# Optimization experiments

Measured on AMD Instinct MI355X. Metric: run time of the kernel, lower is better.

## Reference

```python
import jax, jax.numpy as jnp
import numpy as np

B, S, T = 32, 64, 64          # batch, src_len, tgt_len
E = 1024                      # embedding_dim
H = 512                       # encoder hidden per direction
H2 = 2 * H                    # decoder hidden = enc_output_dim = 1024
VS, VT = 32000, 32000         # src / tgt vocab
L_ENC, L_DEC = 2, 2


def setup_inputs() -> dict:
    key = jax.random.key(0)
    ks = jax.random.split(key, 16)
    s = 0.05
    return {
        # tokens in [1, V) -> no pad tokens, all src_lens == S
        "x": jax.random.randint(ks[0], (B, S), 1, VS),
        "y": jax.random.randint(ks[1], (B, T), 1, VT),
        "src_emb": jax.random.normal(ks[2], (VS, E), jnp.float32) * s,
        "tgt_emb": jax.random.normal(ks[3], (VT, E), jnp.float32) * s,
        # encoder weights: [layer, dir(0=fwd,1=bwd), 4H, in] with in = E = 2H
        "enc_W_ih": jax.random.normal(ks[4], (L_ENC, 2, 4 * H, E), jnp.float32) * s,
        "enc_W_hh": jax.random.normal(ks[5], (L_ENC, 2, 4 * H, H), jnp.float32) * s,
        "enc_b_ih": jax.random.normal(ks[6], (L_ENC, 2, 4 * H), jnp.float32) * s,
        "enc_b_hh": jax.random.normal(ks[7], (L_ENC, 2, 4 * H), jnp.float32) * s,
        # decoder LSTMCells: cell0 input = E + H2 = 2048, cell1 input = H2
        "dec_W_ih0": jax.random.normal(ks[8], (4 * H2, E + H2), jnp.float32) * s,
        "dec_W_ih1": jax.random.normal(ks[9], (4 * H2, H2), jnp.float32) * s,
        "dec_W_hh": jax.random.normal(ks[10], (L_DEC, 4 * H2, H2), jnp.float32) * s,
        "dec_b_ih": jax.random.normal(ks[11], (L_DEC, 4 * H2), jnp.float32) * s,
        "dec_b_hh": jax.random.normal(ks[12], (L_DEC, 4 * H2), jnp.float32) * s,
        "W_out": jax.random.normal(ks[13], (VT, H2), jnp.float32) * s,
        "b_out": jax.random.normal(ks[14], (VT,), jnp.float32) * s,
    }


def _lstm_cell(x, h, c, W_ih, W_hh, b):
    # PyTorch gate order: i, f, g, o
    gates = x @ W_ih.T + h @ W_hh.T + b
    i, f, g, o = jnp.split(gates, 4, axis=-1)
    c2 = jax.nn.sigmoid(f) * c + jax.nn.sigmoid(i) * jnp.tanh(g)
    h2 = jax.nn.sigmoid(o) * jnp.tanh(c2)
    return h2, c2


def _run_dir(xseq, W_ih, W_hh, b):
    # xseq: [T, B, D] -> outputs [T, B, H], final (h, c)
    Bn, Hn = xseq.shape[1], W_hh.shape[1]
    init = (jnp.zeros((Bn, Hn), xseq.dtype), jnp.zeros((Bn, Hn), xseq.dtype))
    def step(carry, xt):
        h, c = carry
        h2, c2 = _lstm_cell(xt, h, c, W_ih, W_hh, b)
        return (h2, c2), h2
    (hT, cT), ys = jax.lax.scan(step, init, xseq)
    return ys, hT, cT


def _forward(x, y, src_emb, tgt_emb, enc_W_ih, enc_W_hh, enc_b_ih, enc_b_hh,
             dec_W_ih0, dec_W_ih1, dec_W_hh, dec_b_ih, dec_b_hh, W_out, b_out):
    # All src lengths are full -> per-row flip == full flip (pack is a no-op).
    x_rev = jnp.flip(x, axis=1)
    seq = src_emb[x_rev].transpose(1, 0, 2)  # [S, B, E]; dropout=0 (eval)

    h_fin, c_fin = [], []
    for l in range(L_ENC):
        b_f = enc_b_ih[l, 0] + enc_b_hh[l, 0]
        b_b = enc_b_ih[l, 1] + enc_b_hh[l, 1]
        ys_f, hT_f, cT_f = _run_dir(seq, enc_W_ih[l, 0], enc_W_hh[l, 0], b_f)
        ys_b, hT_b, cT_b = _run_dir(seq[::-1], enc_W_ih[l, 1], enc_W_hh[l, 1], b_b)
        seq = jnp.concatenate([ys_f, ys_b[::-1]], axis=-1)  # [S, B, 2H]
        h_fin.append(jnp.concatenate([hT_f, hT_b], axis=-1))  # [B, 2H]
        c_fin.append(jnp.concatenate([cT_f, cT_b], axis=-1))

    context = h_fin[-1]  # cat(hidden[-2], hidden[-1]) = last-layer fwd||bwd

    db0 = dec_b_ih[0] + dec_b_hh[0]
    db1 = dec_b_ih[1] + dec_b_hh[1]
    emb_seq = tgt_emb[y[:, :-1]].transpose(1, 0, 2)  # [T-1, B, E] teacher forcing

    def dec_step(carry, emb_t):
        h0, c0, h1, c1 = carry
        inp0 = jnp.concatenate([emb_t, context], axis=-1)
        h0, c0 = _lstm_cell(inp0, h0, c0, dec_W_ih0, dec_W_hh[0], db0)
        h1, c1 = _lstm_cell(h0, h1, c1, dec_W_ih1, dec_W_hh[1], db1)
        logit = h1 @ W_out.T + b_out
        return (h0, c0, h1, c1), logit

    init = (h_fin[0], c_fin[0], h_fin[1], c_fin[1])
    _, logits = jax.lax.scan(dec_step, init, emb_seq)  # [T-1, B, VT]
    return logits.transpose(1, 0, 2)  # [B, T-1, VT]


def reference(x, y, src_emb, tgt_emb, enc_W_ih, enc_W_hh, enc_b_ih, enc_b_hh,
              dec_W_ih0, dec_W_ih1, dec_W_hh, dec_b_ih, dec_b_hh, W_out, b_out):
    return _forward(x, y, src_emb, tgt_emb, enc_W_ih, enc_W_hh, enc_b_ih, enc_b_hh,
                    dec_W_ih0, dec_W_ih1, dec_W_hh, dec_b_ih, dec_b_hh, W_out, b_out)
```

## Files before the change

### kernel.cpp

```cpp
#include <hip/hip_runtime.h>

typedef __attribute__((ext_vector_type(8))) short short8;
typedef __attribute__((ext_vector_type(4))) float f32x4;

#define DEVINL __device__ __forceinline__

DEVINL unsigned short f2bf(float f) {
  unsigned int u = __builtin_bit_cast(unsigned int, f);
  unsigned int r = u + 0x7FFFu + ((u >> 16) & 1u);
  return (unsigned short)(r >> 16);
}
DEVINL float bf2f(unsigned short u) {
  unsigned int x = ((unsigned int)u) << 16;
  return __builtin_bit_cast(float, x);
}
DEVINL float sig_(float x) { return 1.f / (1.f + __expf(-x)); }
DEVINL float tanh_(float x) { return 2.f / (1.f + __expf(-2.f * x)) - 1.f; }

DEVINL void gld16(void* lds, const void* g) {
  __builtin_amdgcn_global_load_lds(
      (const __attribute__((address_space(1))) unsigned int*)g,
      (__attribute__((address_space(3))) unsigned int*)lds, 16, 0, 0);
}

DEVINL void coh_st(unsigned long long* p, unsigned long long v) {
  __hip_atomic_store(p, v, __ATOMIC_RELAXED, __HIP_MEMORY_SCOPE_AGENT);
}

DEVINL unsigned long long pack4w(unsigned int u, int lane, int s0, int s1) {
  unsigned int p1 = (unsigned int)__shfl_xor((int)u, s0);
  unsigned int lo2 = (lane & s0) ? ((p1 & 0xFFFFu) | (u << 16))
                                 : ((u & 0xFFFFu) | (p1 << 16));
  unsigned int p2 = (unsigned int)__shfl_xor((int)lo2, s1);
  unsigned int lo = (lane & s1) ? p2 : lo2;
  unsigned int hi = (lane & s1) ? lo2 : p2;
  return ((unsigned long long)hi << 32) | lo;
}

DEVINL void bar_arrive(int* arr, int idx, int gen) {
  if (threadIdx.x == 0)
    __hip_atomic_store(arr + idx * 16, gen, __ATOMIC_RELAXED, __HIP_MEMORY_SCOPE_AGENT);
}
DEVINL void wait1(const int* arr, int nb, int gen) {
  if (threadIdx.x < 64) {
    for (;;) {
      int ok = 1;
      for (int i = (int)threadIdx.x; i < nb; i += 64)
        ok &= (__hip_atomic_load(arr + i * 16, __ATOMIC_RELAXED,
                                 __HIP_MEMORY_SCOPE_AGENT) >= gen)
                  ? 1
                  : 0;
      if (__all(ok)) break;
      __builtin_amdgcn_s_sleep(2);
    }
  }
  __builtin_amdgcn_sched_barrier(0);
  asm volatile("" ::: "memory");
  __syncthreads();
}
DEVINL void wait2(const int* a0, int n0, int g0, const int* a1, int n1, int g1) {
  if (threadIdx.x < 64) {
    for (;;) {
      int ok = 1;
      for (int i = (int)threadIdx.x; i < n0; i += 64)
        ok &= (__hip_atomic_load(a0 + i * 16, __ATOMIC_RELAXED,
                                 __HIP_MEMORY_SCOPE_AGENT) >= g0)
                  ? 1
                  : 0;
      for (int i = (int)threadIdx.x; i < n1; i += 64)
        ok &= (__hip_atomic_load(a1 + i * 16, __ATOMIC_RELAXED,
                                 __HIP_MEMORY_SCOPE_AGENT) >= g1)
                  ? 1
                  : 0;
      if (__all(ok)) break;
      __builtin_amdgcn_s_sleep(2);
    }
  }
  __builtin_amdgcn_sched_barrier(0);
  asm volatile("" ::: "memory");
  __syncthreads();
}

__global__ __launch_bounds__(256) void gemm_bf16(
    const unsigned short* __restrict__ A, const unsigned short* __restrict__ Bt,
    void* __restrict__ C, const float* __restrict__ bias,
    int K, int N, int Mvalid, int mode) {
  __shared__ unsigned short lA[1024 * 8];
  __shared__ unsigned short lB[1024 * 8];
  const int tid = threadIdx.x;
  const int lane = tid & 63, wid = tid >> 6;
  const int wm = wid >> 1, wn = wid & 1;
  const int bm = blockIdx.x, bn = blockIdx.y;
  const size_t K_ = (size_t)K;

  const unsigned short* gAc[4];
  const unsigned short* gBc[4];
  unsigned short* lAc[4];
  unsigned short* lBc[4];
#pragma unroll
  for (int c = 0; c < 4; c++) {
    const int s = c * 256 + tid;
    const int r = s & 127, kb = s >> 7;
    gAc[c] = A + (size_t)(bm * 128 + r) * K_ + kb * 8;
    gBc[c] = Bt + (size_t)(bn * 128 + r) * K_ + kb * 8;
    lAc[c] = lA + (size_t)(c * 256 + wid * 64) * 8;
    lBc[c] = lB + (size_t)(c * 256 + wid * 64) * 8;
  }

  f32x4 acc[4][4] = {};
  const int kg = lane >> 4, lr = lane & 15;

  for (int kt = 0; kt < K; kt += 64) {
#pragma unroll
    for (int c = 0; c < 4; c++) {
      gld16(lAc[c], gAc[c] + kt);
      gld16(lBc[c], gBc[c] + kt);
    }
    __syncthreads();
#pragma unroll
    for (int ks = 0; ks < 2; ks++) {
      const int kgi = ks * 4 + kg;
      short8 af[4], bfr[4];
#pragma unroll
      for (int fm = 0; fm < 4; fm++)
        af[fm] = *(const short8*)&lA[(size_t)(kgi * 128 + wm * 64 + fm * 16 + lr) * 8];
#pragma unroll
      for (int fn = 0; fn < 4; fn++)
        bfr[fn] = *(const short8*)&lB[(size_t)(kgi * 128 + wn * 64 + fn * 16 + lr) * 8];
#pragma unroll
      for (int fm = 0; fm < 4; fm++)
#pragma unroll
        for (int fn = 0; fn < 4; fn++)
          acc[fm][fn] =
              __builtin_amdgcn_mfma_f32_16x16x32_bf16(af[fm], bfr[fn], acc[fm][fn], 0, 0, 0);
    }
    __syncthreads();
  }

#pragma unroll
  for (int fn = 0; fn < 4; fn++) {
    const int col = bn * 128 + wn * 64 + fn * 16 + lr;
    const float bv = bias ? bias[col] : 0.f;
#pragma unroll
    for (int fm = 0; fm < 4; fm++) {
      const int row0 = bm * 128 + wm * 64 + fm * 16 + kg * 4;
#pragma unroll
      for (int r = 0; r < 4; r++) {
        const int m = row0 + r;
        if (m < Mvalid) {
          const float v = acc[fm][fn][r] + bv;
          if (mode == 0) {
            ((float*)C)[(size_t)m * N + col] = v;
          } else if (mode == 1) {
            const int b = m & 31, t = m >> 5;
            ((float*)C)[(size_t)b * 2016000 + (size_t)t * 32000 + col] = v;
          } else {
            ((unsigned short*)C)[(size_t)m * N + col] = f2bf(v);
          }
        }
      }
    }
  }
}

__global__ __launch_bounds__(128, 1) void enc_chain(
    const unsigned short* __restrict__ Whh, const unsigned short* __restrict__ G,
    unsigned short* __restrict__ Henc, unsigned short* __restrict__ seq_out,
    float* __restrict__ c_out, int* bar) {
  extern __shared__ unsigned short lw[];
  const int tid = threadIdx.x, lane = tid & 63, w = tid >> 6;
  const int lr = lane & 15, kg = lane >> 4;
  const int dir = (int)blockIdx.x >> 4, j0 = ((int)blockIdx.x & 15) * 32;
  int* arr = bar + dir * 256;
  const int aidx = (int)blockIdx.x & 15;
  const unsigned short* Wd = Whh + (size_t)dir * 2048 * 512;
  for (int it = 0; it < 64; it++) {
    const int idx = (it * 128 + tid) * 16;
    const int r = idx >> 10, o = idx & 1023;
    const unsigned short* src = Wd + (size_t)((r >> 5) * 512 + j0 + (r & 31)) * 512 + (o >> 1);
    *(short8*)((char*)lw + r * 1024 + (o ^ ((r & 7) << 4))) = *(const short8*)src;
  }
  float cc[2][4] = {};
  float gpre[4][2][4];
  auto fetch_g = [&](int t) {
    const int s_idx = dir ? (63 - t) : t;
#pragma unroll
    for (int r = 0; r < 4; r++) {
      const unsigned short* Gr =
          G + (size_t)(s_idx * 32 + (w * 16 + kg * 4 + r)) * 4096 + dir * 2048;
#pragma unroll
      for (int jh = 0; jh < 2; jh++) {
        const int jj = j0 + jh * 16 + lr;
        gpre[r][jh][0] = bf2f(Gr[jj]);
        gpre[r][jh][1] = bf2f(Gr[512 + jj]);
        gpre[r][jh][2] = bf2f(Gr[1024 + jj]);
        gpre[r][jh][3] = bf2f(Gr[1536 + jj]);
      }
    }
  };
  fetch_g(0);
  __syncthreads();
  for (int t = 0; t < 64; t++) {
    const unsigned short* hA =
        Henc + ((size_t)(t * 2 + dir) * 32 + w * 16 + lr) * 512 + kg * 8;
    short8 areg[16];
#pragma unroll
    for (int kc = 0; kc < 16; kc++) areg[kc] = *(const short8*)(hA + kc * 32);
    f32x4 acc[8] = {};
#pragma unroll
    for (int kc = 0; kc < 16; kc++)
#pragma unroll
      for (int nt = 0; nt < 8; nt++) {
        const int rr = nt * 16 + lr;
        short8 bf = *(const short8*)((const char*)lw + rr * 1024 +
                                     ((kc * 64 + kg * 16) ^ ((rr & 7) << 4)));
        acc[nt] = __builtin_amdgcn_mfma_f32_16x16x32_bf16(areg[kc], bf, acc[nt], 0, 0, 0);
      }
    const int s_idx = dir ? (63 - t) : t;
    unsigned long long* HWU =
        (unsigned long long*)Henc + ((size_t)((t + 1) * 2 + dir) * 32) * 128;
#pragma unroll
    for (int r = 0; r < 4; r++) {
      const int b = w * 16 + kg * 4 + r;
#pragma unroll
      for (int jh = 0; jh < 2; jh++) {
        const float gi = gpre[r][jh][0] + acc[jh + 0][r];
        const float gf = gpre[r][jh][1] + acc[jh + 2][r];
        const float gg = gpre[r][jh][2] + acc[jh + 4][r];
        const float go = gpre[r][jh][3] + acc[jh + 6][r];
        const float cn = sig_(gf) * cc[jh][r] + sig_(gi) * tanh_(gg);
        const float hn = sig_(go) * tanh_(cn);
        cc[jh][r] = cn;
        unsigned long long pk = pack4w((unsigned int)f2bf(hn), lane, 1, 2);
        if ((lane & 3) == 0) {
          const int jjb = j0 + jh * 16 + lr;
          coh_st(HWU + b * 128 + (jjb >> 2), pk);
          if (seq_out)
            *(unsigned long long*)&seq_out[(size_t)(s_idx * 32 + b) * 1024 + dir * 512 +
                                           jjb] = pk;
        }
      }
    }
    if (t < 63) {
      __syncthreads();
      bar_arrive(arr, aidx, t + 1);
      fetch_g(t + 1);
      wait1(arr, 16, t + 1);
    }
  }
#pragma unroll
  for (int r = 0; r < 4; r++)
#pragma unroll
    for (int jh = 0; jh < 2; jh++)
      c_out[(dir * 32 + (w * 16 + kg * 4 + r)) * 512 + j0 + jh * 16 + lr] = cc[jh][r];
}

__global__ __launch_bounds__(256, 1) void dec_pipe(
    const unsigned short* __restrict__ Whh0, const unsigned short* __restrict__ Wc1,
    const unsigned short* __restrict__ G, const float* __restrict__ db1,
    const float* __restrict__ c0init, const float* __restrict__ c1init,
    unsigned short* __restrict__ H0ext, unsigned short* __restrict__ H1ext,
    int* arr0, int* arr1) {
  extern __shared__ unsigned short lw[];
  f32x4* red4 = (f32x4*)((char*)lw + 131072);
  const int tid = threadIdx.x, lane = tid & 63;
  const int lr = lane & 15, kg = lane >> 4;
  const int wv = (tid >> 6) & 1, half = tid >> 7;
  const int bid = (int)blockIdx.x;

  if (bid < 64) {
    const int j0 = bid * 16, j = j0 + lr;
    for (int it = 0; it < 32; it++) {
      const int idx = (it * 256 + tid) * 16;
      const int r = idx >> 11, o = idx & 2047;
      const unsigned short* src =
          Whh0 + (size_t)((r >> 4) * 1024 + j0 + (r & 15)) * 1024 + (o >> 1);
      *(short8*)((char*)lw + r * 2048 + (o ^ ((r & 7) << 4))) = *(const short8*)src;
    }
    float cc[4] = {};
    float gpre[4][4];
    auto fetch_g = [&](int k) {
#pragma unroll
      for (int r = 0; r < 4; r++) {
        const unsigned short* Gr = G + (size_t)(k * 32 + (wv * 16 + kg * 4 + r)) * 4096 + j;
        gpre[r][0] = bf2f(Gr[0]);
        gpre[r][1] = bf2f(Gr[1024]);
        gpre[r][2] = bf2f(Gr[2048]);
        gpre[r][3] = bf2f(Gr[3072]);
      }
    };
    if (tid < 128) {
#pragma unroll
      for (int r = 0; r < 4; r++) cc[r] = c0init[(wv * 16 + kg * 4 + r) * 1024 + j];
      fetch_g(0);
    }
    __syncthreads();
    for (int k = 0; k < 63; k++) {
      if (k > 0) wait1(arr0, 64, k);
      const unsigned short* hA =
          H0ext + ((size_t)k * 32 + wv * 16 + lr) * 1024 + half * 512 + kg * 8;
      short8 areg[16];
#pragma unroll
      for (int kcl = 0; kcl < 16; kcl++) areg[kcl] = *(const short8*)(hA + kcl * 32);
      f32x4 acc[4] = {};
#pragma unroll
      for (int kcl = 0; kcl < 16; kcl++) {
        const int kc = half * 16 + kcl;
#pragma unroll
        for (int g = 0; g < 4; g++) {
          const int rr = g * 16 + lr;
          short8 bf = *(const short8*)((const char*)lw + rr * 2048 +
                                       ((kc * 64 + kg * 16) ^ ((rr & 7) << 4)));
          acc[g] = __builtin_amdgcn_mfma_f32_16x16x32_bf16(areg[kcl], bf, acc[g], 0, 0, 0);
        }
      }
      if (half == 1) {
#pragma unroll
        for (int g = 0; g < 4; g++) red4[g * 128 + wv * 64 + lane] = acc[g];
      }
      __syncthreads();
      if (tid < 128) {
        unsigned long long* HWU = (unsigned long long*)H0ext + ((size_t)(k + 1) * 32) * 256;
#pragma unroll
        for (int r = 0; r < 4; r++) {
          const int b = wv * 16 + kg * 4 + r;
          f32x4 a0 = red4[0 * 128 + wv * 64 + lane];
          f32x4 a1 = red4[1 * 128 + wv * 64 + lane];
          f32x4 a2 = red4[2 * 128 + wv * 64 + lane];
          f32x4 a3 = red4[3 * 128 + wv * 64 + lane];
          const float gi = gpre[r][0] + acc[0][r] + a0[r];
          const float gf = gpre[r][1] + acc[1][r] + a1[r];
          const float gg = gpre[r][2] + acc[2][r] + a2[r];
          const float go = gpre[r][3] + acc[3][r] + a3[r];
          const float cn = sig_(gf) * cc[r] + sig_(gi) * tanh_(gg);
          const float hn = sig_(go) * tanh_(cn);
          cc[r] = cn;
          unsigned long long pk = pack4w((unsigned int)f2bf(hn), lane, 1, 2);
          if ((lane & 3) == 0)
            coh_st(HWU + b * 256 + ((j0 + lr) >> 2), pk);
        }
      }
      __syncthreads();
      bar_arrive(arr0, bid, k + 1);
      if (tid < 128 && k < 62) fetch_g(k + 1);
    }
  } else {
    const int j0 = (bid - 64) * 8;
    for (int it = 0; it < 32; it++) {
      const int idx = (it * 256 + tid) * 16;
      const int r = idx >> 12, o = idx & 4095;
      const unsigned short* src =
          Wc1 + (size_t)((r & 3) * 1024 + j0 + (r >> 2)) * 2048 + (o >> 1);
      *(short8*)((char*)lw + r * 4096 + (o ^ ((r & 7) << 4))) = *(const short8*)src;
    }
    float cc[2][4] = {};
    float bb1[2][4] = {};
    if (tid < 128) {
#pragma unroll
      for (int n = 0; n < 2; n++) {
        const int j = j0 + n * 4 + (lr >> 2);
#pragma unroll
        for (int g = 0; g < 4; g++) bb1[n][g] = db1[g * 1024 + j];
#pragma unroll
        for (int r = 0; r < 4; r++)
          cc[n][r] = c1init[(wv * 16 + kg * 4 + r) * 1024 + j];
      }
    }
    __syncthreads();
    for (int t = 0; t < 63; t++) {
      wait2(arr0, 64, t + 1, arr1, 128, t);
      const unsigned short* hA =
          half ? (H1ext + ((size_t)t * 32 + wv * 16 + lr) * 1024 + kg * 8)
               : (H0ext + ((size_t)(t + 1) * 32 + wv * 16 + lr) * 1024 + kg * 8);
      short8 areg[32];
#pragma unroll
      for (int kcl = 0; kcl < 32; kcl++) areg[kcl] = *(const short8*)(hA + kcl * 32);
      f32x4 acc[2] = {};
#pragma unroll
      for (int kcl = 0; kcl < 32; kcl++) {
        const int kc = half * 32 + kcl;
#pragma unroll
        for (int n = 0; n < 2; n++) {
          const int rr = n * 16 + lr;
          short8 bf = *(const short8*)((const char*)lw + rr * 4096 +
                                       ((kc * 64 + kg * 16) ^ ((rr & 7) << 4)));
          acc[n] = __builtin_amdgcn_mfma_f32_16x16x32_bf16(areg[kcl], bf, acc[n], 0, 0, 0);
        }
      }
      if (half == 1) {
#pragma unroll
        for (int n = 0; n < 2; n++) red4[n * 128 + wv * 64 + lane] = acc[n];
      }
      __syncthreads();
      if (tid < 128) {
        unsigned long long* HWU = (unsigned long long*)H1ext + ((size_t)(t + 1) * 32) * 256;
#pragma unroll
        for (int n = 0; n < 2; n++) {
          f32x4 ar = red4[n * 128 + wv * 64 + lane];
#pragma unroll
          for (int r = 0; r < 4; r++) {
            const int b = wv * 16 + kg * 4 + r;
            const float v = acc[n][r] + ar[r];
            const float e1a = __shfl_xor(v, 1);
            const float e0 = (lane & 1) ? e1a : v;
            const float e1 = (lane & 1) ? v : e1a;
            const float f0 = __shfl_xor(e0, 2), f1 = __shfl_xor(e1, 2);
            const float gi = ((lane & 2) ? f0 : e0) + bb1[n][0];
            const float gf = ((lane & 2) ? f1 : e1) + bb1[n][1];
            const float gg = ((lane & 2) ? e0 : f0) + bb1[n][2];
            const float go = ((lane & 2) ? e1 : f1) + bb1[n][3];
            const float cn = sig_(gf) * cc[n][r] + sig_(gi) * tanh_(gg);
            const float hn = sig_(go) * tanh_(cn);
            cc[n][r] = cn;
            unsigned long long pk = pack4w((unsigned int)f2bf(hn), lane, 4, 8);
            if ((lane & 15) == 0)
              coh_st(HWU + b * 256 + ((j0 + n * 4) >> 2), pk);
          }
        }
      }
      __syncthreads();
      bar_arrive(arr1, bid - 64, t + 1);
    }
  }
}

__global__ void cvt_bf16(const float* __restrict__ in, unsigned short* __restrict__ out,
                         long n4) {
  long i = (long)blockIdx.x * blockDim.x + threadIdx.x;
  const long stride = (long)gridDim.x * blockDim.x;
  for (; i < n4; i += stride) {
    f32x4 v = *(const f32x4*)&in[i * 4];
    ushort4 o = {f2bf(v.x), f2bf(v.y), f2bf(v.z), f2bf(v.w)};
    *(ushort4*)&out[i * 4] = o;
  }
}

__global__ void pack_wc1(const float* __restrict__ Wih1, const float* __restrict__ Whh1,
                         unsigned short* __restrict__ Wc) {
  const int n = blockIdx.x;
  const int c = threadIdx.x * 8;
  const float* src = (c < 1024) ? (Wih1 + (size_t)n * 1024 + c)
                                : (Whh1 + (size_t)n * 1024 + (c - 1024));
  f32x4 v0 = *(const f32x4*)src;
  f32x4 v1 = *(const f32x4*)(src + 4);
  ushort4 o0 = {f2bf(v0.x), f2bf(v0.y), f2bf(v0.z), f2bf(v0.w)};
  ushort4 o1 = {f2bf(v1.x), f2bf(v1.y), f2bf(v1.z), f2bf(v1.w)};
  *(ushort4*)&Wc[(size_t)n * 2048 + c] = o0;
  *(ushort4*)&Wc[(size_t)n * 2048 + c + 4] = o1;
}

__global__ void bias_comb(const float* __restrict__ a, const float* __restrict__ b,
                          float* __restrict__ out, int n) {
  int i = blockIdx.x * blockDim.x + threadIdx.x;
  if (i < n) out[i] = a[i] + b[i];
}

__global__ void embed_src(const int* __restrict__ x, const float* __restrict__ emb,
                          unsigned short* __restrict__ A0) {
  const int row = blockIdx.x;
  const int s = row >> 5, b = row & 31;
  const int tok = x[b * 64 + (63 - s)];
  const int col = threadIdx.x * 4;
  f32x4 v = *(const f32x4*)(emb + (size_t)tok * 1024 + col);
  ushort4 o = {f2bf(v.x), f2bf(v.y), f2bf(v.z), f2bf(v.w)};
  *(ushort4*)&A0[(size_t)row * 1024 + col] = o;
}

__global__ void embed_tgt(const int* __restrict__ y, const float* __restrict__ emb,
                          unsigned short* __restrict__ inp0) {
  const int row = blockIdx.x;
  const int col = threadIdx.x * 4;
  ushort4 o = {0, 0, 0, 0};
  if (row < 2016) {
    const int t = row >> 5, b = row & 31;
    const int tok = y[b * 64 + t];
    f32x4 v = *(const f32x4*)(emb + (size_t)tok * 1024 + col);
    o = ushort4{f2bf(v.x), f2bf(v.y), f2bf(v.z), f2bf(v.w)};
  } else {
    *(ushort4*)&inp0[(size_t)row * 2048 + 1024 + col] = o;
  }
  *(ushort4*)&inp0[(size_t)row * 2048 + col] = o;
}

__global__ void fill_ctx2(const unsigned short* __restrict__ Hl1,
                          unsigned short* __restrict__ inp0) {
  const int row = blockIdx.x;
  const int b = row & 31;
  const int col = threadIdx.x * 4;
  const int dir = col >> 9, jj = col & 511;
  ushort4 v = *(const ushort4*)(Hl1 + ((size_t)dir * 32 + b) * 512 + jj);
  *(ushort4*)&inp0[(size_t)row * 2048 + 1024 + col] = v;
}

__global__ void dec_init2(const unsigned short* __restrict__ Hl0,
                          const unsigned short* __restrict__ Hl1,
                          const float* __restrict__ Cl0, const float* __restrict__ Cl1,
                          unsigned short* __restrict__ H0e, unsigned short* __restrict__ H1e,
                          float* __restrict__ c0, float* __restrict__ c1) {
  const int i = blockIdx.x * 256 + threadIdx.x;
  const int b = i >> 10, col = i & 1023;
  const int dir = col >> 9, jj = col & 511;
  const int se = (dir * 32 + b) * 512 + jj;
  const int de = b * 1024 + col;
  H0e[de] = Hl0[se];
  H1e[de] = Hl1[se];
  c0[de] = Cl0[se];
  c1[de] = Cl1[se];
}

extern "C" void kernel_launch(void* const* d_in, const int* in_sizes, int n_in,
                              void* d_out, int out_size, void* d_ws, size_t ws_size,
                              hipStream_t stream) {
  const int* x = (const int*)d_in[0];
  const int* y = (const int*)d_in[1];
  const float* src_emb = (const float*)d_in[2];
  const float* tgt_emb = (const float*)d_in[3];
  const float* enc_W_ih = (const float*)d_in[4];
  const float* enc_W_hh = (const float*)d_in[5];
  const float* enc_b_ih = (const float*)d_in[6];
  const float* enc_b_hh = (const float*)d_in[7];
  const float* dec_W_ih0 = (const float*)d_in[8];
  const float* dec_W_ih1 = (const float*)d_in[9];
  const float* dec_W_hh = (const float*)d_in[10];
  const float* dec_b_ih = (const float*)d_in[11];
  const float* dec_b_hh = (const float*)d_in[12];
  const float* W_out = (const float*)d_in[13];
  const float* b_out = (const float*)d_in[14];
  float* out = (float*)d_out;

  char* ws = (char*)d_ws;
  size_t off = 0;
  auto alloc = [&](size_t bytes) -> void* {
    void* p = ws + off;
    off += (bytes + 255) & ~(size_t)255;
    return p;
  };
  unsigned short* A0 = (unsigned short*)alloc(2048ull * 1024 * 2);
  unsigned short* seq1 = (unsigned short*)alloc(2048ull * 1024 * 2);
  unsigned short* Wih_bf = (unsigned short*)alloc(2ull * 4096 * 1024 * 2);
  unsigned short* Wih0_bf = (unsigned short*)alloc(4096ull * 2048 * 2);
  unsigned short* Wout_bf = (unsigned short*)alloc(32000ull * 1024 * 2);
  unsigned short* G = (unsigned short*)alloc(2048ull * 4096 * 2);
  unsigned short* inp0 = (unsigned short*)alloc(2048ull * 2048 * 2);
  unsigned short* Whh_enc_bf = (unsigned short*)alloc(2ull * 2 * 2048 * 512 * 2);
  unsigned short* Whh0_bf = (unsigned short*)alloc(4096ull * 1024 * 2);
  unsigned short* Wc1_bf = (unsigned short*)alloc(4096ull * 2048 * 2);
  unsigned short* H0ext = (unsigned short*)alloc(2080ull * 1024 * 2);
  unsigned short* H1ext = (unsigned short*)alloc(2080ull * 1024 * 2);
  unsigned short* Henc0 = (unsigned short*)alloc(65ull * 2 * 32 * 512 * 2);
  unsigned short* Henc1 = (unsigned short*)alloc(65ull * 2 * 32 * 512 * 2);
  float* encbias = (float*)alloc(2ull * 4096 * 4);
  float* decdb = (float*)alloc(2ull * 4096 * 4);
  float* c_l0 = (float*)alloc(2ull * 32 * 512 * 4);
  float* c_l1 = (float*)alloc(2ull * 32 * 512 * 4);
  float* c0buf = (float*)alloc(32ull * 1024 * 4);
  float* c1buf = (float*)alloc(32ull * 1024 * 4);
  int* bar = (int*)alloc(4096 * 4);
  if (off > ws_size) return;

  (void)hipFuncSetAttribute((const void*)enc_chain,
                            hipFuncAttributeMaxDynamicSharedMemorySize, 131072);
  (void)hipFuncSetAttribute((const void*)dec_pipe,
                            hipFuncAttributeMaxDynamicSharedMemorySize, 139264);

  cvt_bf16<<<1024, 256, 0, stream>>>(enc_W_ih, Wih_bf, (2ll * 4096 * 1024) / 4);
  cvt_bf16<<<1024, 256, 0, stream>>>(dec_W_ih0, Wih0_bf, (4096ll * 2048) / 4);
  cvt_bf16<<<2048, 256, 0, stream>>>(W_out, Wout_bf, (32000ll * 1024) / 4);
  cvt_bf16<<<1024, 256, 0, stream>>>(enc_W_hh, Whh_enc_bf, (2ll * 2 * 2048 * 512) / 4);
  cvt_bf16<<<1024, 256, 0, stream>>>(dec_W_hh, Whh0_bf, (4096ll * 1024) / 4);
  pack_wc1<<<4096, 256, 0, stream>>>(dec_W_ih1, dec_W_hh + 4096ll * 1024, Wc1_bf);
  bias_comb<<<32, 256, 0, stream>>>(enc_b_ih, enc_b_hh, encbias, 8192);
  bias_comb<<<32, 256, 0, stream>>>(dec_b_ih, dec_b_hh, decdb, 8192);
  embed_src<<<2048, 256, 0, stream>>>(x, src_emb, A0);
  embed_tgt<<<2048, 256, 0, stream>>>(y, tgt_emb, inp0);
  hipMemsetAsync(Henc0, 0, 2ull * 32 * 512 * 2, stream);
  hipMemsetAsync(Henc1, 0, 2ull * 32 * 512 * 2, stream);
  hipMemsetAsync(bar, 0, 4096 * 4, stream);

  gemm_bf16<<<dim3(16, 32), 256, 0, stream>>>(A0, Wih_bf, G, encbias, 1024, 4096, 2048, 2);
  enc_chain<<<32, 128, 131072, stream>>>(Whh_enc_bf, G, Henc0, seq1, c_l0, bar + 0);
  gemm_bf16<<<dim3(16, 32), 256, 0, stream>>>(seq1, Wih_bf + 4096ull * 1024, G,
                                              encbias + 4096, 1024, 4096, 2048, 2);
  enc_chain<<<32, 128, 131072, stream>>>(Whh_enc_bf + 2ull * 2048 * 512, G, Henc1, nullptr,
                                         c_l1, bar + 512);

  dec_init2<<<128, 256, 0, stream>>>(Henc0 + 64ull * 2 * 32 * 512,
                                     Henc1 + 64ull * 2 * 32 * 512, c_l0, c_l1,
                                     H0ext, H1ext, c0buf, c1buf);
  fill_ctx2<<<2016, 256, 0, stream>>>(Henc1 + 64ull * 2 * 32 * 512, inp0);
  gemm_bf16<<<dim3(16, 32), 256, 0, stream>>>(inp0, Wih0_bf, G, decdb, 2048, 4096, 2048, 2);

  dec_pipe<<<192, 256, 139264, stream>>>(Whh0_bf, Wc1_bf, G, decdb + 4096, c0buf, c1buf,
                                         H0ext, H1ext, bar + 1024, bar + 2048);

  gemm_bf16<<<dim3(16, 250), 256, 0, stream>>>(H1ext + 32ull * 1024, Wout_bf, out, b_out,
                                               1024, 32000, 2016, 1);
}
```

Baseline: 2.163 ms.

## Split encoder recurrence K across waves, decouple decoder waits, fuse setup kernels

The encoder recurrent kernel now runs 256 threads per block, splitting the K dimension of the h·W_hh product across two halves and reducing partial sums through extra shared memory. In the decoder pipeline, the wave half that reads the layer-1 hidden state no longer waits for the layer-0 flag, so only the layer-0 half polls per wave. Separately, the eight weight-conversion and bias kernels are merged into one grid-stride setup kernel to cut launch count. These changes trade an extra barrier and LDS reduction per encoder step for shorter serial MFMA chains, and add a per-wave polling path in the decoder.

```diff
diff --git a/kernel.cpp b/kernel.cpp
--- a/kernel.cpp
+++ b/kernel.cpp
@@ -58,27 +58,20 @@
   asm volatile("" ::: "memory");
   __syncthreads();
 }
-DEVINL void wait2(const int* a0, int n0, int g0, const int* a1, int n1, int g1) {
-  if (threadIdx.x < 64) {
-    for (;;) {
-      int ok = 1;
-      for (int i = (int)threadIdx.x; i < n0; i += 64)
-        ok &= (__hip_atomic_load(a0 + i * 16, __ATOMIC_RELAXED,
-                                 __HIP_MEMORY_SCOPE_AGENT) >= g0)
-                  ? 1
-                  : 0;
-      for (int i = (int)threadIdx.x; i < n1; i += 64)
-        ok &= (__hip_atomic_load(a1 + i * 16, __ATOMIC_RELAXED,
-                                 __HIP_MEMORY_SCOPE_AGENT) >= g1)
-                  ? 1
-                  : 0;
-      if (__all(ok)) break;
-      __builtin_amdgcn_s_sleep(2);
-    }
+DEVINL void wave_poll_arr(const int* arr, int nb, int gen) {
+  const int lane = (int)threadIdx.x & 63;
+  for (;;) {
+    int ok = 1;
+    for (int i = lane; i < nb; i += 64)
+      ok &= (__hip_atomic_load(arr + i * 16, __ATOMIC_RELAXED,
+                               __HIP_MEMORY_SCOPE_AGENT) >= gen)
+                ? 1
+                : 0;
+    if (__all(ok)) break;
+    __builtin_amdgcn_s_sleep(2);
   }
   __builtin_amdgcn_sched_barrier(0);
   asm volatile("" ::: "memory");
-  __syncthreads();
 }
 
 __global__ __launch_bounds__(256) void gemm_bf16(
@@ -163,19 +156,21 @@
   }
 }
 
-__global__ __launch_bounds__(128, 1) void enc_chain(
+__global__ __launch_bounds__(256, 1) void enc_chain(
     const unsigned short* __restrict__ Whh, const unsigned short* __restrict__ G,
     unsigned short* __restrict__ Henc, unsigned short* __restrict__ seq_out,
     float* __restrict__ c_out, int* bar) {
   extern __shared__ unsigned short lw[];
-  const int tid = threadIdx.x, lane = tid & 63, w = tid >> 6;
+  f32x4* red8 = (f32x4*)((char*)lw + 131072);
+  const int tid = threadIdx.x, lane = tid & 63;
   const int lr = lane & 15, kg = lane >> 4;
+  const int wv = (tid >> 6) & 1, half = tid >> 7;
   const int dir = (int)blockIdx.x >> 4, j0 = ((int)blockIdx.x & 15) * 32;
   int* arr = bar + dir * 256;
   const int aidx = (int)blockIdx.x & 15;
   const unsigned short* Wd = Whh + (size_t)dir * 2048 * 512;
-  for (int it = 0; it < 64; it++) {
-    const int idx = (it * 128 + tid) * 16;
+  for (int it = 0; it < 32; it++) {
+    const int idx = (it * 256 + tid) * 16;
     const int r = idx >> 10, o = idx & 1023;
     const unsigned short* src = Wd + (size_t)((r >> 5) * 512 + j0 + (r & 31)) * 512 + (o >> 1);
     *(short8*)((char*)lw + r * 1024 + (o ^ ((r & 7) << 4))) = *(const short8*)src;
@@ -187,7 +182,7 @@
 #pragma unroll
     for (int r = 0; r < 4; r++) {
       const unsigned short* Gr =
-          G + (size_t)(s_idx * 32 + (w * 16 + kg * 4 + r)) * 4096 + dir * 2048;
+          G + (size_t)(s_idx * 32 + (wv * 16 + kg * 4 + r)) * 4096 + dir * 2048;
 #pragma unroll
       for (int jh = 0; jh < 2; jh++) {
         const int jj = j0 + jh * 16 + lr;
@@ -198,61 +193,78 @@
       }
     }
   };
-  fetch_g(0);
+  if (tid < 128) fetch_g(0);
   __syncthreads();
   for (int t = 0; t < 64; t++) {
     const unsigned short* hA =
-        Henc + ((size_t)(t * 2 + dir) * 32 + w * 16 + lr) * 512 + kg * 8;
-    short8 areg[16];
-#pragma unroll
-    for (int kc = 0; kc < 16; kc++) areg[kc] = *(const short8*)(hA + kc * 32);
+        Henc + ((size_t)(t * 2 + dir) * 32 + wv * 16 + lr) * 512 + half * 256 + kg * 8;
+    short8 areg[8];
+#pragma unroll
+    for (int kcl = 0; kcl < 8; kcl++) areg[kcl] = *(const short8*)(hA + kcl * 32);
     f32x4 acc[8] = {};
 #pragma unroll
-    for (int kc = 0; kc < 16; kc++)
+    for (int kcl = 0; kcl < 8; kcl++) {
+      const int kc = half * 8 + kcl;
 #pragma unroll
       for (int nt = 0; nt < 8; nt++) {
         const int rr = nt * 16 + lr;
         short8 bf = *(const short8*)((const char*)lw + rr * 1024 +
                                      ((kc * 64 + kg * 16) ^ ((rr & 7) << 4)));
-        acc[nt] = __builtin_amdgcn_mfma_f32_16x16x32_bf16(areg[kc], bf, acc[nt], 0, 0, 0);
-      }
-    const int s_idx = dir ? (63 - t) : t;
-    unsigned long long* HWU =
-        (unsigned long long*)Henc + ((size_t)((t + 1) * 2 + dir) * 32) * 128;
-#pragma unroll
-    for (int r = 0; r < 4; r++) {
-      const int b = w * 16 + kg * 4 + r;
-#pragma unroll
-      for (int jh = 0; jh < 2; jh++) {
-        const float gi = gpre[r][jh][0] + acc[jh + 0][r];
-        const float gf = gpre[r][jh][1] + acc[jh + 2][r];
-        const float gg = gpre[r][jh][2] + acc[jh + 4][r];
-        const float go = gpre[r][jh][3] + acc[jh + 6][r];
-        const float cn = sig_(gf) * cc[jh][r] + sig_(gi) * tanh_(gg);
-        const float hn = sig_(go) * tanh_(cn);
-        cc[jh][r] = cn;
-        unsigned long long pk = pack4w((unsigned int)f2bf(hn), lane, 1, 2);
-        if ((lane & 3) == 0) {
-          const int jjb = j0 + jh * 16 + lr;
-          coh_st(HWU + b * 128 + (jjb >> 2), pk);
-          if (seq_out)
-            *(unsigned long long*)&seq_out[(size_t)(s_idx * 32 + b) * 1024 + dir * 512 +
-                                           jjb] = pk;
+        acc[nt] = __builtin_amdgcn_mfma_f32_16x16x32_bf16(areg[kcl], bf, acc[nt], 0, 0, 0);
+      }
+    }
+    if (half == 1) {
+#pragma unroll
+      for (int nt = 0; nt < 8; nt++) red8[nt * 128 + wv * 64 + lane] = acc[nt];
+    }
+    __syncthreads();
+    if (tid < 128) {
+      const int s_idx = dir ? (63 - t) : t;
+      unsigned long long* HWU =
+          (unsigned long long*)Henc + ((size_t)((t + 1) * 2 + dir) * 32) * 128;
+#pragma unroll
+      for (int nt = 0; nt < 8; nt++) {
+        f32x4 ar = red8[nt * 128 + wv * 64 + lane];
+        acc[nt][0] += ar[0]; acc[nt][1] += ar[1];
+        acc[nt][2] += ar[2]; acc[nt][3] += ar[3];
+      }
+#pragma unroll
+      for (int r = 0; r < 4; r++) {
+        const int b = wv * 16 + kg * 4 + r;
+#pragma unroll
+        for (int jh = 0; jh < 2; jh++) {
+          const float gi = gpre[r][jh][0] + acc[jh + 0][r];
+          const float gf = gpre[r][jh][1] + acc[jh + 2][r];
+          const float gg = gpre[r][jh][2] + acc[jh + 4][r];
+          const float go = gpre[r][jh][3] + acc[jh + 6][r];
+          const float cn = sig_(gf) * cc[jh][r] + sig_(gi) * tanh_(gg);
+          const float hn = sig_(go) * tanh_(cn);
+          cc[jh][r] = cn;
+          unsigned long long pk = pack4w((unsigned int)f2bf(hn), lane, 1, 2);
+          if ((lane & 3) == 0) {
+            const int jjb = j0 + jh * 16 + lr;
+            coh_st(HWU + b * 128 + (jjb >> 2), pk);
+            if (seq_out)
+              *(unsigned long long*)&seq_out[(size_t)(s_idx * 32 + b) * 1024 + dir * 512 +
+                                             jjb] = pk;
+          }
         }
       }
     }
     if (t < 63) {
       __syncthreads();
       bar_arrive(arr, aidx, t + 1);
-      fetch_g(t + 1);
+      if (tid < 128) fetch_g(t + 1);
       wait1(arr, 16, t + 1);
     }
   }
-#pragma unroll
-  for (int r = 0; r < 4; r++)
-#pragma unroll
-    for (int jh = 0; jh < 2; jh++)
-      c_out[(dir * 32 + (w * 16 + kg * 4 + r)) * 512 + j0 + jh * 16 + lr] = cc[jh][r];
+  if (tid < 128) {
+#pragma unroll
+    for (int r = 0; r < 4; r++)
+#pragma unroll
+      for (int jh = 0; jh < 2; jh++)
+        c_out[(dir * 32 + (wv * 16 + kg * 4 + r)) * 512 + j0 + jh * 16 + lr] = cc[jh][r];
+  }
 }
 
 __global__ __launch_bounds__(256, 1) void dec_pipe(
@@ -368,23 +380,41 @@
     }
     __syncthreads();
     for (int t = 0; t < 63; t++) {
-      wait2(arr0, 64, t + 1, arr1, 128, t);
-      const unsigned short* hA =
-          half ? (H1ext + ((size_t)t * 32 + wv * 16 + lr) * 1024 + kg * 8)
-               : (H0ext + ((size_t)(t + 1) * 32 + wv * 16 + lr) * 1024 + kg * 8);
-      short8 areg[32];
-#pragma unroll
-      for (int kcl = 0; kcl < 32; kcl++) areg[kcl] = *(const short8*)(hA + kcl * 32);
+      wait1(arr1, 128, t);
       f32x4 acc[2] = {};
-#pragma unroll
-      for (int kcl = 0; kcl < 32; kcl++) {
-        const int kc = half * 32 + kcl;
-#pragma unroll
-        for (int n = 0; n < 2; n++) {
-          const int rr = n * 16 + lr;
-          short8 bf = *(const short8*)((const char*)lw + rr * 4096 +
-                                       ((kc * 64 + kg * 16) ^ ((rr & 7) << 4)));
-          acc[n] = __builtin_amdgcn_mfma_f32_16x16x32_bf16(areg[kcl], bf, acc[n], 0, 0, 0);
+      {
+        short8 areg[32];
+        if (half) {
+          const unsigned short* hA = H1ext + ((size_t)t * 32 + wv * 16 + lr) * 1024 + kg * 8;
+#pragma unroll
+          for (int kcl = 0; kcl < 32; kcl++) areg[kcl] = *(const short8*)(hA + kcl * 32);
+#pragma unroll
+          for (int kcl = 0; kcl < 32; kcl++) {
+            const int kc = 32 + kcl;
+#pragma unroll
+            for (int n = 0; n < 2; n++) {
+              const int rr = n * 16 + lr;
+              short8 bf = *(const short8*)((const char*)lw + rr * 4096 +
+                                           ((kc * 64 + kg * 16) ^ ((rr & 7) << 4)));
+              acc[n] = __builtin_amdgcn_mfma_f32_16x16x32_bf16(areg[kcl], bf, acc[n], 0, 0, 0);
+            }
+          }
+        } else {
+          wave_poll_arr(arr0, 64, t + 1);
+          const unsigned short* hA =
+              H0ext + ((size_t)(t + 1) * 32 + wv * 16 + lr) * 1024 + kg * 8;
+#pragma unroll
+          for (int kcl = 0; kcl < 32; kcl++) areg[kcl] = *(const short8*)(hA + kcl * 32);
+#pragma unroll
+          for (int kcl = 0; kcl < 32; kcl++) {
+#pragma unroll
+            for (int n = 0; n < 2; n++) {
+              const int rr = n * 16 + lr;
+              short8 bf = *(const short8*)((const char*)lw + rr * 4096 +
+                                           ((kcl * 64 + kg * 16) ^ ((rr & 7) << 4)));
+              acc[n] = __builtin_amdgcn_mfma_f32_16x16x32_bf16(areg[kcl], bf, acc[n], 0, 0, 0);
+            }
+          }
         }
       }
       if (half == 1) {
@@ -424,35 +454,55 @@
   }
 }
 
-__global__ void cvt_bf16(const float* __restrict__ in, unsigned short* __restrict__ out,
-                         long n4) {
-  long i = (long)blockIdx.x * blockDim.x + threadIdx.x;
+struct SetupPtrs {
+  const float *encWih, *encWhh, *decWih0, *decWhh, *decWih1, *Wout;
+  unsigned short *WihBf, *WhhEncBf, *Wih0Bf, *Whh0Bf, *Wc1Bf, *WoutBf;
+  const float *encBa, *encBb;
+  float* encBd;
+  const float *decBa, *decBb;
+  float* decBd;
+};
+
+__global__ void setup_all(SetupPtrs p) {
+  const long e0 = 2097152, e1 = e0 + 1048576, e2 = e1 + 2097152, e3 = e2 + 1048576;
+  const long e4 = e3 + 2097152, e5 = e4 + 8192000, e6 = e5 + 2048, e7 = e6 + 2048;
   const long stride = (long)gridDim.x * blockDim.x;
-  for (; i < n4; i += stride) {
-    f32x4 v = *(const f32x4*)&in[i * 4];
-    ushort4 o = {f2bf(v.x), f2bf(v.y), f2bf(v.z), f2bf(v.w)};
-    *(ushort4*)&out[i * 4] = o;
-  }
-}
-
-__global__ void pack_wc1(const float* __restrict__ Wih1, const float* __restrict__ Whh1,
-                         unsigned short* __restrict__ Wc) {
-  const int n = blockIdx.x;
-  const int c = threadIdx.x * 8;
-  const float* src = (c < 1024) ? (Wih1 + (size_t)n * 1024 + c)
-                                : (Whh1 + (size_t)n * 1024 + (c - 1024));
-  f32x4 v0 = *(const f32x4*)src;
-  f32x4 v1 = *(const f32x4*)(src + 4);
-  ushort4 o0 = {f2bf(v0.x), f2bf(v0.y), f2bf(v0.z), f2bf(v0.w)};
-  ushort4 o1 = {f2bf(v1.x), f2bf(v1.y), f2bf(v1.z), f2bf(v1.w)};
-  *(ushort4*)&Wc[(size_t)n * 2048 + c] = o0;
-  *(ushort4*)&Wc[(size_t)n * 2048 + c + 4] = o1;
-}
-
-__global__ void bias_comb(const float* __restrict__ a, const float* __restrict__ b,
-                          float* __restrict__ out, int n) {
-  int i = blockIdx.x * blockDim.x + threadIdx.x;
-  if (i < n) out[i] = a[i] + b[i];
+  for (long i = (long)blockIdx.x * blockDim.x + threadIdx.x; i < e7; i += stride) {
+    if (i < e5) {
+      const float* s;
+      unsigned short* d;
+      long k;
+      if (i < e0) { s = p.encWih; d = p.WihBf; k = i; }
+      else if (i < e1) { s = p.encWhh; d = p.WhhEncBf; k = i - e0; }
+      else if (i < e2) { s = p.decWih0; d = p.Wih0Bf; k = i - e1; }
+      else if (i < e3) { s = p.decWhh; d = p.Whh0Bf; k = i - e2; }
+      else if (i < e4) {
+        k = i - e3;
+        const long n = k >> 9, c = (k & 511) * 4;
+        const float* src = (c < 1024) ? (p.decWih1 + n * 1024 + c)
+                                      : (p.decWhh + 4096l * 1024 + n * 1024 + (c - 1024));
+        f32x4 v = *(const f32x4*)src;
+        ushort4 o = {f2bf(v.x), f2bf(v.y), f2bf(v.z), f2bf(v.w)};
+        *(ushort4*)&p.Wc1Bf[k * 4] = o;
+        continue;
+      } else { s = p.Wout; d = p.WoutBf; k = i - e4; }
+      f32x4 v = *(const f32x4*)&s[k * 4];
+      ushort4 o = {f2bf(v.x), f2bf(v.y), f2bf(v.z), f2bf(v.w)};
+      *(ushort4*)&d[k * 4] = o;
+    } else if (i < e6) {
+      const long k = i - e5;
+      f32x4 a = *(const f32x4*)&p.encBa[k * 4];
+      f32x4 b = *(const f32x4*)&p.encBb[k * 4];
+      f32x4 o = {a.x + b.x, a.y + b.y, a.z + b.z, a.w + b.w};
+      *(f32x4*)&p.encBd[k * 4] = o;
+    } else {
+      const long k = i - e6;
+      f32x4 a = *(const f32x4*)&p.decBa[k * 4];
+      f32x4 b = *(const f32x4*)&p.decBb[k * 4];
+      f32x4 o = {a.x + b.x, a.y + b.y, a.z + b.z, a.w + b.w};
+      *(f32x4*)&p.decBd[k * 4] = o;
+    }
+  }
 }
 
 __global__ void embed_src(const int* __restrict__ x, const float* __restrict__ emb,
@@ -559,18 +609,18 @@
   if (off > ws_size) return;
 
   (void)hipFuncSetAttribute((const void*)enc_chain,
-                            hipFuncAttributeMaxDynamicSharedMemorySize, 131072);
+                            hipFuncAttributeMaxDynamicSharedMemorySize, 147456);
   (void)hipFuncSetAttribute((const void*)dec_pipe,
                             hipFuncAttributeMaxDynamicSharedMemorySize, 139264);
 
-  cvt_bf16<<<1024, 256, 0, stream>>>(enc_W_ih, Wih_bf, (2ll * 4096 * 1024) / 4);
-  cvt_bf16<<<1024, 256, 0, stream>>>(dec_W_ih0, Wih0_bf, (4096ll * 2048) / 4);
-  cvt_bf16<<<2048, 256, 0, stream>>>(W_out, Wout_bf, (32000ll * 1024) / 4);
-  cvt_bf16<<<1024, 256, 0, stream>>>(enc_W_hh, Whh_enc_bf, (2ll * 2 * 2048 * 512) / 4);
-  cvt_bf16<<<1024, 256, 0, stream>>>(dec_W_hh, Whh0_bf, (4096ll * 1024) / 4);
-  pack_wc1<<<4096, 256, 0, stream>>>(dec_W_ih1, dec_W_hh + 4096ll * 1024, Wc1_bf);
-  bias_comb<<<32, 256, 0, stream>>>(enc_b_ih, enc_b_hh, encbias, 8192);
-  bias_comb<<<32, 256, 0, stream>>>(dec_b_ih, dec_b_hh, decdb, 8192);
+  SetupPtrs sp;
+  sp.encWih = enc_W_ih; sp.encWhh = enc_W_hh; sp.decWih0 = dec_W_ih0;
+  sp.decWhh = dec_W_hh; sp.decWih1 = dec_W_ih1; sp.Wout = W_out;
+  sp.WihBf = Wih_bf; sp.WhhEncBf = Whh_enc_bf; sp.Wih0Bf = Wih0_bf;
+  sp.Whh0Bf = Whh0_bf; sp.Wc1Bf = Wc1_bf; sp.WoutBf = Wout_bf;
+  sp.encBa = enc_b_ih; sp.encBb = enc_b_hh; sp.encBd = encbias;
+  sp.decBa = dec_b_ih; sp.decBb = dec_b_hh; sp.decBd = decdb;
+  setup_all<<<2048, 256, 0, stream>>>(sp);
   embed_src<<<2048, 256, 0, stream>>>(x, src_emb, A0);
   embed_tgt<<<2048, 256, 0, stream>>>(y, tgt_emb, inp0);
   hipMemsetAsync(Henc0, 0, 2ull * 32 * 512 * 2, stream);
@@ -578,10 +628,10 @@
   hipMemsetAsync(bar, 0, 4096 * 4, stream);
 
   gemm_bf16<<<dim3(16, 32), 256, 0, stream>>>(A0, Wih_bf, G, encbias, 1024, 4096, 2048, 2);
-  enc_chain<<<32, 128, 131072, stream>>>(Whh_enc_bf, G, Henc0, seq1, c_l0, bar + 0);
+  enc_chain<<<32, 256, 147456, stream>>>(Whh_enc_bf, G, Henc0, seq1, c_l0, bar + 0);
   gemm_bf16<<<dim3(16, 32), 256, 0, stream>>>(seq1, Wih_bf + 4096ull * 1024, G,
                                               encbias + 4096, 1024, 4096, 2048, 2);
-  enc_chain<<<32, 128, 131072, stream>>>(Whh_enc_bf + 2ull * 2048 * 512, G, Henc1, nullptr,
+  enc_chain<<<32, 256, 147456, stream>>>(Whh_enc_bf + 2ull * 2048 * 512, G, Henc1, nullptr,
                                          c_l1, bar + 512);
 
   dec_init2<<<128, 256, 0, stream>>>(Henc0 + 64ull * 2 * 32 * 512,
```

Result: faster. 2.077 ms (-4.0%).
